# Kernel tuning notes

Measured on AMD Instinct MI355X. Metric: run time of the kernel, lower is better.

## Reference

```python
import jax, jax.numpy as jnp
import numpy as np

N = 100000   # nodes
F = 512      # in_channels
H = 128      # hidden_channels
HEADS = 2
E = 1600000  # edges
C = 64       # out_channels (classes)
EPS = 1e-5
GW = 0.8     # graph_weight


def setup_inputs() -> dict:
    key = jax.random.key(0)
    ks = jax.random.split(key, 16)
    rn = lambda k, s: jax.random.normal(k, s, jnp.float32) * 0.05
    return {
        'x': jax.random.normal(ks[0], (N, F), jnp.float32),
        'edge_index': jax.random.randint(ks[1], (2, E), 0, N),
        # TransConv params
        't_fc_w': rn(ks[2], (F, H)), 't_fc_b': jnp.zeros((H,), jnp.float32),
        't_ln0_g': jnp.ones((H,), jnp.float32), 't_ln0_b': jnp.zeros((H,), jnp.float32),
        't_wq_w': rn(ks[3], (H, H * HEADS)), 't_wq_b': jnp.zeros((H * HEADS,), jnp.float32),
        't_wk_w': rn(ks[4], (H, H * HEADS)), 't_wk_b': jnp.zeros((H * HEADS,), jnp.float32),
        't_wv_w': rn(ks[5], (H, H * HEADS)), 't_wv_b': jnp.zeros((H * HEADS,), jnp.float32),
        't_ln1_g': jnp.ones((H,), jnp.float32), 't_ln1_b': jnp.zeros((H,), jnp.float32),
        # GraphConv params
        'g_fc_w': rn(ks[6], (F, H)), 'g_fc_b': jnp.zeros((H,), jnp.float32),
        'g_bn0_g': jnp.ones((H,), jnp.float32), 'g_bn0_b': jnp.zeros((H,), jnp.float32),
        'g_conv_w': rn(ks[7], (H, H)), 'g_conv_b': jnp.zeros((H,), jnp.float32),
        'g_bn1_g': jnp.ones((H,), jnp.float32), 'g_bn1_b': jnp.zeros((H,), jnp.float32),
        # output fc
        'fc_w': rn(ks[8], (H, C)), 'fc_b': jnp.zeros((C,), jnp.float32),
    }


def _layernorm(x, g, b):
    mu = jnp.mean(x, axis=-1, keepdims=True)
    var = jnp.mean((x - mu) ** 2, axis=-1, keepdims=True)
    return (x - mu) * jax.lax.rsqrt(var + EPS) * g + b


def _batchnorm_eval(x, g, b):
    # eval-mode BN right after reset: running_mean=0, running_var=1
    return x * (1.0 / np.sqrt(1.0 + EPS)) * g + b


def _trans_conv(x, fc_w, fc_b, ln0_g, ln0_b, wq_w, wq_b, wk_w, wk_b, wv_w, wv_b, ln1_g, ln1_b):
    h = jax.nn.relu(_layernorm(x @ fc_w + fc_b, ln0_g, ln0_b))
    x0 = h
    n = h.shape[0]
    qs = (h @ wq_w + wq_b).reshape(n, HEADS, H)
    ks = (h @ wk_w + wk_b).reshape(n, HEADS, H)
    vs = (h @ wv_w + wv_b).reshape(n, HEADS, H)
    # global (Frobenius) norm, as in torch.norm(qs, p=2)
    qs = qs / jnp.linalg.norm(qs)
    ks = ks / jnp.linalg.norm(ks)
    kvs = jnp.einsum('lhm,lhd->hmd', ks, vs)                  # [h, m, d]
    attention_num = jnp.einsum('nhm,hmd->nhd', qs, kvs) + n * vs
    ks_sum = jnp.sum(ks, axis=0)                              # [h, m]
    normalizer = jnp.einsum('nhm,hm->nh', qs, ks_sum)[..., None] + float(n)
    attn_out = (attention_num / normalizer).mean(axis=1)       # [n, H]
    h = (attn_out + x0) / 2.0
    h = jax.nn.relu(_layernorm(h, ln1_g, ln1_b))
    return h


def _graph_conv(x, edge_index, fc_w, fc_b, bn0_g, bn0_b, conv_w, conv_b, bn1_g, bn1_b):
    h = jax.nn.relu(_batchnorm_eval(x @ fc_w + fc_b, bn0_g, bn0_b))
    x0 = h
    row, col = edge_index[0], edge_index[1]
    n = h.shape[0]
    deg = jax.ops.segment_sum(jnp.ones((row.shape[0],), jnp.float32), col, num_segments=n)
    val = jnp.sqrt(1.0 / deg[col]) * jnp.sqrt(1.0 / deg[row])
    val = jnp.nan_to_num(val, nan=0.0, posinf=0.0, neginf=0.0)
    agg = jax.ops.segment_sum(val[:, None] * h[row], col, num_segments=n)  # [n, H]
    h2 = agg @ conv_w + conv_b
    h2 = jax.nn.relu(_batchnorm_eval(h2, bn1_g, bn1_b))
    return h2 + x0


def reference(x, edge_index,
              t_fc_w, t_fc_b, t_ln0_g, t_ln0_b, t_wq_w, t_wq_b, t_wk_w, t_wk_b,
              t_wv_w, t_wv_b, t_ln1_g, t_ln1_b,
              g_fc_w, g_fc_b, g_bn0_g, g_bn0_b, g_conv_w, g_conv_b, g_bn1_g, g_bn1_b,
              fc_w, fc_b):
    x1 = _trans_conv(x, t_fc_w, t_fc_b, t_ln0_g, t_ln0_b, t_wq_w, t_wq_b,
                     t_wk_w, t_wk_b, t_wv_w, t_wv_b, t_ln1_g, t_ln1_b)
    x2 = _graph_conv(x, edge_index, g_fc_w, g_fc_b, g_bn0_g, g_bn0_b,
                     g_conv_w, g_conv_b, g_bn1_g, g_bn1_b)
    out = GW * x2 + (1.0 - GW) * x1
    return out @ fc_w + fc_b
```

## Files before the change

kernel.cpp:

```cpp
#include <hip/hip_runtime.h>

constexpr int N = 100000;
constexpr int F = 512;
constexpr int H = 128;
constexpr int E = 1600000;
constexpr int C = 64;
constexpr float EPS = 1e-5f;
constexpr float NF = 100000.0f;
constexpr float IBN = 0.999995000037f;

constexpr size_t OFF_HT   = 0;
constexpr size_t OFF_HG   = 12800000;
constexpr size_t OFF_AGG  = 25600000;
constexpr size_t OFF_CNT  = 38400000;
constexpr size_t OFF_S    = 38500000;
constexpr size_t OFF_G    = 38500128;
constexpr size_t OFF_PTR  = 38516512;
constexpr size_t OFF_CUR  = 38616512;
constexpr size_t OFF_BS   = 38716512;
constexpr size_t OFF_SROW = 38716640;
constexpr size_t OFF_SVAL = 40316640;
constexpr size_t OFF_GWV  = 41916640;
constexpr size_t OFF_KV   = OFF_GWV + 3 * 32768;
constexpr size_t OFF_KSUM = OFF_KV + 32768;
constexpr size_t OFF_VSUM = OFF_KSUM + 256;
constexpr size_t OFF_QSUM = OFF_VSUM + 256;
constexpr size_t OFF_SC   = OFF_QSUM + 256;
constexpr size_t OFF_B    = OFF_SC + 4;
constexpr size_t OFF_CC   = OFF_B + 32768;
constexpr size_t OFF_U    = OFF_CC + 256;
constexpr size_t OFF_U0   = OFF_U + 256;
constexpr size_t OFF_BT   = OFF_U0 + 4;

constexpr int NB1024 = (N + 1023) / 1024;
constexpr int NB_GRAM = (N + 255) / 256;
constexpr size_t SP_BASE = (size_t)NB_GRAM * 16384;

typedef __attribute__((ext_vector_type(8))) short short8;
typedef __attribute__((ext_vector_type(4))) float floatx4;

__device__ __forceinline__ float4 ld4(const float* p) {
  return *reinterpret_cast<const float4*>(p);
}
__device__ __forceinline__ void st4(float* p, float4 v) {
  *reinterpret_cast<float4*>(p) = v;
}
__device__ __forceinline__ unsigned short f2bf(float f) {
  unsigned u = __float_as_uint(f);
  u += 0x7fff + ((u >> 16) & 1);
  return (unsigned short)(u >> 16);
}
__device__ __forceinline__ float bf2f(unsigned short h) {
  return __uint_as_float((unsigned)h << 16);
}
__device__ __forceinline__ void gl_lds16(const unsigned short* g, unsigned short* l) {
  __builtin_amdgcn_global_load_lds(
      (const __attribute__((address_space(1))) unsigned int*)g,
      (__attribute__((address_space(3))) unsigned int*)l, 16, 0, 0);
}

__global__ __launch_bounds__(256) void k0_cvt(const float* __restrict__ Wt,
    const float* __restrict__ Wg, unsigned short* __restrict__ Bt)
{
  const int idx = blockIdx.x * 256 + threadIdx.x;
  const int k = idx >> 8;
  const int n = idx & 255;
  float v = (n < 128) ? Wt[(size_t)k * H + n] : Wg[(size_t)k * H + (n - 128)];
  const int kt = k >> 5;
  const int g  = (k >> 3) & 3;
  const int e  = k & 7;
  const int chunk = g * 256 + ((n + 2 * g) & 255);
  Bt[(((size_t)kt * 1024 + chunk) << 3) + e] = f2bf(v);
}

__global__ __launch_bounds__(256, 3) void k1_mfma(
    const float* __restrict__ x, const unsigned short* __restrict__ Bt,
    const float* __restrict__ bt, const float* __restrict__ lng, const float* __restrict__ lnb,
    const float* __restrict__ bgv, const float* __restrict__ bng, const float* __restrict__ bnb,
    float* __restrict__ ht, float* __restrict__ hg)
{
  __shared__ __align__(16) union {
    struct { unsigned short A[2][64 * 40]; unsigned short B[2][8192]; } st;
    struct { float lns[64 * 132]; float mu[64]; float rs[64]; } ln;
  } sm;
  const int t = threadIdx.x;
  const int lane = t & 63;
  const int w = t >> 6;
  const int rq = (w >> 1) * 32;
  const int cq = (w & 1) * 128;
  const int g = lane >> 4;
  const int m = lane & 15;
  const int M0 = blockIdx.x * 64;

  floatx4 acc[2][8];
#pragma unroll
  for (int rt = 0; rt < 2; ++rt)
#pragma unroll
    for (int ct = 0; ct < 8; ++ct) acc[rt][ct] = (floatx4){0.f, 0.f, 0.f, 0.f};

  const int srow = t >> 2;
  const int scol8 = (t & 3) * 8;
  const int grow = (M0 + srow < N) ? (M0 + srow) : (N - 1);
  const float* xp = x + (size_t)grow * F + scol8;

  const int mb = cq + m + 2 * g;

  {
#pragma unroll
    for (int i = 0; i < 4; ++i)
      gl_lds16(Bt + (((size_t)(i * 256 + t)) << 3),
               &sm.st.B[0][(size_t)(i * 256 + (w << 6)) << 3]);
    float4 a0 = ld4(xp), a1 = ld4(xp + 4);
    ushort4 p0, p1;
    p0.x = f2bf(a0.x); p0.y = f2bf(a0.y); p0.z = f2bf(a0.z); p0.w = f2bf(a0.w);
    p1.x = f2bf(a1.x); p1.y = f2bf(a1.y); p1.z = f2bf(a1.z); p1.w = f2bf(a1.w);
    *(ushort4*)(sm.st.A[0] + srow * 40 + scol8) = p0;
    *(ushort4*)(sm.st.A[0] + srow * 40 + scol8 + 4) = p1;
  }
  __syncthreads();

#pragma unroll 2
  for (int kt = 0; kt < 16; ++kt) {
    const int cur = kt & 1, nxt = cur ^ 1;
    float4 a0, a1;
    const bool more = (kt + 1 < 16);
    if (more) {
#pragma unroll
      for (int i = 0; i < 4; ++i)
        gl_lds16(Bt + (((size_t)(kt + 1) * 1024 + i * 256 + t) << 3),
                 &sm.st.B[nxt][(size_t)(i * 256 + (w << 6)) << 3]);
      a0 = ld4(xp + (kt + 1) * 32);
      a1 = ld4(xp + (kt + 1) * 32 + 4);
    }
    {
      const unsigned short* Ab = sm.st.A[cur];
      const unsigned short* Bb = sm.st.B[cur];
      short8 af[2], bf[8];
#pragma unroll
      for (int rt = 0; rt < 2; ++rt)
        af[rt] = *(const short8*)(Ab + (rq + rt * 16 + m) * 40 + g * 8);
#pragma unroll
      for (int ct = 0; ct < 8; ++ct) {
        const int chunk = g * 256 + ((mb + ct * 16) & 255);
        bf[ct] = *(const short8*)(Bb + ((size_t)chunk << 3));
      }
#pragma unroll
      for (int rt = 0; rt < 2; ++rt)
#pragma unroll
        for (int ct = 0; ct < 8; ++ct)
          acc[rt][ct] = __builtin_amdgcn_mfma_f32_16x16x32_bf16(af[rt], bf[ct], acc[rt][ct], 0, 0, 0);
    }
    if (more) {
      ushort4 p0, p1;
      p0.x = f2bf(a0.x); p0.y = f2bf(a0.y); p0.z = f2bf(a0.z); p0.w = f2bf(a0.w);
      p1.x = f2bf(a1.x); p1.y = f2bf(a1.y); p1.z = f2bf(a1.z); p1.w = f2bf(a1.w);
      *(ushort4*)(sm.st.A[nxt] + srow * 40 + scol8) = p0;
      *(ushort4*)(sm.st.A[nxt] + srow * 40 + scol8 + 4) = p1;
    }
    __syncthreads();
  }

  if (cq == 0) {
#pragma unroll
    for (int rt = 0; rt < 2; ++rt)
#pragma unroll
      for (int ct = 0; ct < 8; ++ct) {
        const int col = ct * 16 + m;
        const float b = bt[col];
#pragma unroll
        for (int r = 0; r < 4; ++r)
          sm.ln.lns[(rq + rt * 16 + g * 4 + r) * 132 + col] = acc[rt][ct][r] + b;
      }
  } else {
#pragma unroll
    for (int rt = 0; rt < 2; ++rt)
#pragma unroll
      for (int ct = 0; ct < 8; ++ct) {
        const int col = ct * 16 + m;
        const float s1 = IBN * bng[col], b0 = bgv[col], b2 = bnb[col];
#pragma unroll
        for (int r = 0; r < 4; ++r) {
          const int row = M0 + rq + rt * 16 + g * 4 + r;
          if (row < N) {
            float v = (acc[rt][ct][r] + b0) * s1 + b2;
            hg[(size_t)row * H + col] = v > 0.f ? v : 0.f;
          }
        }
      }
  }
  __syncthreads();
  if (t < 64) {
    float sum = 0.f, sq = 0.f;
    for (int c2 = 0; c2 < H; ++c2) {
      float v = sm.ln.lns[t * 132 + c2];
      sum += v; sq += v * v;
    }
    float mu = sum * (1.f / H);
    float var = sq * (1.f / H) - mu * mu;
    sm.ln.mu[t] = mu; sm.ln.rs[t] = rsqrtf(var + EPS);
  }
  __syncthreads();
  {
    const int r = t >> 2;
    const int cb = (t & 3) * 32;
    if (M0 + r < N) {
      const float mu = sm.ln.mu[r], rs = sm.ln.rs[r];
#pragma unroll
      for (int j = 0; j < 8; ++j) {
        const int c = cb + j * 4;
        float o[4];
#pragma unroll
        for (int q = 0; q < 4; ++q) {
          float v = (sm.ln.lns[r * 132 + c + q] - mu) * rs * lng[c + q] + lnb[c + q];
          o[q] = v > 0.f ? v : 0.f;
        }
        st4(ht + (size_t)(M0 + r) * H + c, make_float4(o[0], o[1], o[2], o[3]));
      }
    }
  }
}

__global__ __launch_bounds__(256) void k2_gram(const float* __restrict__ ht,
                                               float* __restrict__ gp,
                                               float* __restrict__ sp)
{
  const int t = threadIdx.x;
  const int b = blockIdx.x;
  const int base = b * 256;
  const int nend = (base + 256 < N) ? base + 256 : N;
  const int r0 = (t >> 4) * 8;
  const int c0 = (t & 15) * 8;
  float acc[8][8] = {};
  float colacc[8] = {};
  const bool do_col = (t < 16);
  int n = base;
  for (; n + 1 < nend; n += 2) {
    const float* hp0 = ht + (size_t)n * H;
    const float* hp1 = hp0 + H;
    float4 a00 = ld4(hp0 + r0), a01 = ld4(hp0 + r0 + 4);
    float4 b00 = ld4(hp0 + c0), b01 = ld4(hp0 + c0 + 4);
    float4 a10 = ld4(hp1 + r0), a11 = ld4(hp1 + r0 + 4);
    float4 b10 = ld4(hp1 + c0), b11 = ld4(hp1 + c0 + 4);
    float a0[8] = {a00.x, a00.y, a00.z, a00.w, a01.x, a01.y, a01.z, a01.w};
    float b0[8] = {b00.x, b00.y, b00.z, b00.w, b01.x, b01.y, b01.z, b01.w};
    float a1[8] = {a10.x, a10.y, a10.z, a10.w, a11.x, a11.y, a11.z, a11.w};
    float b1[8] = {b10.x, b10.y, b10.z, b10.w, b11.x, b11.y, b11.z, b11.w};
    if (do_col) {
#pragma unroll
      for (int j = 0; j < 8; ++j) colacc[j] += b0[j] + b1[j];
    }
#pragma unroll
    for (int i = 0; i < 8; ++i)
#pragma unroll
      for (int j = 0; j < 8; ++j)
        acc[i][j] += a0[i] * b0[j] + a1[i] * b1[j];
  }
  if (n < nend) {
    const float* hp0 = ht + (size_t)n * H;
    float4 a00 = ld4(hp0 + r0), a01 = ld4(hp0 + r0 + 4);
    float4 b00 = ld4(hp0 + c0), b01 = ld4(hp0 + c0 + 4);
    float a0[8] = {a00.x, a00.y, a00.z, a00.w, a01.x, a01.y, a01.z, a01.w};
    float b0[8] = {b00.x, b00.y, b00.z, b00.w, b01.x, b01.y, b01.z, b01.w};
    if (do_col) {
#pragma unroll
      for (int j = 0; j < 8; ++j) colacc[j] += b0[j];
    }
#pragma unroll
    for (int i = 0; i < 8; ++i)
#pragma unroll
      for (int j = 0; j < 8; ++j)
        acc[i][j] += a0[i] * b0[j];
  }
  float* g = gp + (size_t)b * 16384;
#pragma unroll
  for (int i = 0; i < 8; ++i) {
    st4(&g[(r0 + i) * H + c0], make_float4(acc[i][0], acc[i][1], acc[i][2], acc[i][3]));
    st4(&g[(r0 + i) * H + c0 + 4], make_float4(acc[i][4], acc[i][5], acc[i][6], acc[i][7]));
  }
  if (do_col) {
    float* spb = sp + (size_t)b * 128;
    st4(&spb[c0], make_float4(colacc[0], colacc[1], colacc[2], colacc[3]));
    st4(&spb[c0 + 4], make_float4(colacc[4], colacc[5], colacc[6], colacc[7]));
  }
}

__global__ __launch_bounds__(256) void k2r_reduce(const float* __restrict__ gp,
    const float* __restrict__ sp, float* __restrict__ G, float* __restrict__ s)
{
  const int i = blockIdx.x * 256 + threadIdx.x;
  float s0 = 0.f, s1 = 0.f, s2 = 0.f, s3 = 0.f;
  int b = 0;
  for (; b + 3 < NB_GRAM; b += 4) {
    s0 += gp[(size_t)b * 16384 + i];
    s1 += gp[(size_t)(b + 1) * 16384 + i];
    s2 += gp[(size_t)(b + 2) * 16384 + i];
    s3 += gp[(size_t)(b + 3) * 16384 + i];
  }
  for (; b < NB_GRAM; ++b) s0 += gp[(size_t)b * 16384 + i];
  G[i] = (s0 + s1) + (s2 + s3);
  if (blockIdx.x == 0 && threadIdx.x < 128) {
    float t0 = 0.f, t1 = 0.f;
    int bb = 0;
    for (; bb + 1 < NB_GRAM; bb += 2) {
      t0 += sp[(size_t)bb * 128 + threadIdx.x];
      t1 += sp[(size_t)(bb + 1) * 128 + threadIdx.x];
    }
    for (; bb < NB_GRAM; ++bb) t0 += sp[(size_t)bb * 128 + threadIdx.x];
    s[threadIdx.x] = t0 + t1;
  }
}

__global__ __launch_bounds__(256) void k3a_gw(const float* __restrict__ G,
    const float* __restrict__ Wv, const float* __restrict__ Wk,
    const float* __restrict__ Wq, float* __restrict__ GW)
{
  const int flat = blockIdx.x * 256 + threadIdx.x;
  const int w = flat >> 15;
  const int rem = flat & 32767;
  const int i = rem >> 8;
  const int j = rem & 255;
  const float* W = (w == 0) ? Wv : (w == 1) ? Wk : Wq;
  float sum = 0.f;
#pragma unroll 8
  for (int k = 0; k < H; ++k) sum += G[i * H + k] * W[k * 256 + j];
  GW[flat] = sum;
}

__global__ __launch_bounds__(256) void k3k_sums(const float* __restrict__ s,
    const float* __restrict__ Wk, const float* __restrict__ bk,
    const float* __restrict__ Wv, const float* __restrict__ bv,
    const float* __restrict__ Wq, const float* __restrict__ bq,
    float* __restrict__ ksum, float* __restrict__ vsum, float* __restrict__ qsum)
{
  const int flat = blockIdx.x * 256 + threadIdx.x;
  const int w = flat >> 8;
  const int j = flat & 255;
  const float* W = (w == 0) ? Wk : (w == 1) ? Wv : Wq;
  const float* b = (w == 0) ? bk : (w == 1) ? bv : bq;
  float* out = (w == 0) ? ksum : (w == 1) ? vsum : qsum;
  float sum = 0.f;
#pragma unroll 8
  for (int k = 0; k < H; ++k) sum += s[k] * W[k * 256 + j];
  out[j] = sum + NF * b[j];
}

__global__ __launch_bounds__(256) void k3b_kv(const float* __restrict__ GWv,
    const float* __restrict__ s, const float* __restrict__ Wk,
    const float* __restrict__ bk, const float* __restrict__ bv,
    const float* __restrict__ vsum, float* __restrict__ kv)
{
  const int flat = blockIdx.x * 256 + threadIdx.x;
  const int h = flat >> 14;
  const int m = (flat >> 7) & 127;
  const int d = flat & 127;
  float s1 = 0.f, s2 = 0.f;
#pragma unroll 4
  for (int k = 0; k < H; ++k) {
    float wkv = Wk[k * 256 + h * 128 + m];
    s1 += wkv * GWv[k * 256 + h * 128 + d];
    s2 += wkv * s[k];
  }
  kv[flat] = s1 + s2 * bv[h * 128 + d] + bk[h * 128 + m] * vsum[h * 128 + d];
}

__global__ __launch_bounds__(256) void k3c_ssq(
    const float* __restrict__ Wk, const float* __restrict__ GWk,
    const float* __restrict__ Wq, const float* __restrict__ GWq,
    const float* __restrict__ bk, const float* __restrict__ ksum,
    const float* __restrict__ bq, const float* __restrict__ qsum,
    float* __restrict__ sc)
{
  __shared__ float red[512];
  const int t = threadIdx.x;
  float pk = 0.f, pq = 0.f;
  for (int i = t; i < 32768; i += 256) {
    pk += Wk[i] * GWk[i];
    pq += Wq[i] * GWq[i];
  }
  pk += 2.f * bk[t] * ksum[t] - NF * bk[t] * bk[t];
  pq += 2.f * bq[t] * qsum[t] - NF * bq[t] * bq[t];
  red[t] = pk; red[256 + t] = pq;
  __syncthreads();
  for (int off = 128; off > 0; off >>= 1) {
    if (t < off) { red[t] += red[t + off]; red[256 + t] += red[256 + t + off]; }
    __syncthreads();
  }
  if (t == 0) {
    float ssq_k = red[0], ssq_q = red[256];
    sc[0] = ssq_q; sc[1] = ssq_k;
    sc[2] = rsqrtf(ssq_q * ssq_k);
  }
}

__global__ __launch_bounds__(256) void k3d_B(const float* __restrict__ Wq,
    const float* __restrict__ kv, const float* __restrict__ Wv,
    const float* __restrict__ sc, unsigned short* __restrict__ Bt2)
{
  const int flat = blockIdx.x * 256 + threadIdx.x;
  const int i = flat >> 8;
  const int j = flat & 255;
  const int h = j >> 7;
  const int d = j & 127;
  const float inv = sc[2];
  float sum = 0.f;
#pragma unroll 4
  for (int m = 0; m < H; ++m)
    sum += Wq[i * 256 + h * 128 + m] * kv[h * 16384 + m * 128 + d];
  Bt2[(size_t)j * H + i] = f2bf(sum * inv + NF * Wv[i * 256 + j]);
}

__global__ __launch_bounds__(512) void k3e_small(const float* __restrict__ bq,
    const float* __restrict__ kv, const float* __restrict__ bv,
    const float* __restrict__ Wq, const float* __restrict__ ksum,
    const float* __restrict__ sc, float* __restrict__ cc,
    float* __restrict__ u, float* __restrict__ u0)
{
  const int t = threadIdx.x;
  const float inv = sc[2];
  if (t < 256) {
    const int h = t >> 7, d = t & 127;
    float sum = 0.f;
    for (int m = 0; m < H; ++m) sum += bq[h * 128 + m] * kv[h * 16384 + m * 128 + d];
    cc[t] = sum * inv + NF * bv[t];
  } else {
    const int q = t - 256;
    const int i = q >> 1, h = q & 1;
    float sum = 0.f;
    for (int m = 0; m < H; ++m) sum += Wq[i * 256 + h * 128 + m] * ksum[h * 128 + m];
    u[i * 2 + h] = sum * inv;
  }
  if (t < 2) {
    float sum = 0.f;
    for (int m = 0; m < H; ++m) sum += bq[t * 128 + m] * ksum[t * 128 + m];
    u0[t] = sum * inv + NF;
  }
}

__global__ __launch_bounds__(256) void k4_mfma(float* __restrict__ ht,
    const unsigned short* __restrict__ Bt2, const float* __restrict__ cc,
    const float* __restrict__ u, const float* __restrict__ u0,
    const float* __restrict__ lng, const float* __restrict__ lnb)
{
  __shared__ __align__(16) union {
    unsigned short A[64 * 136];
    float lns[64 * 132];
  } sm;
  __shared__ float u_s[256];
  __shared__ float rden_s[128];
  __shared__ float mu_s[64], rs_s[64];
  const int t = threadIdx.x;
  const int lane = t & 63;
  const int w = t >> 6;
  const int rq = w * 16;
  const int g = lane >> 4;
  const int m = lane & 15;
  const int M0 = blockIdx.x * 64;

  {
    const int srow = t >> 2;
    const int scol = (t & 3) * 32;
    const int grow = (M0 + srow < N) ? (M0 + srow) : (N - 1);
    const float* xp = ht + (size_t)grow * H + scol;
#pragma unroll
    for (int j = 0; j < 8; ++j) {
      float4 a4 = ld4(xp + j * 4);
      ushort4 p;
      p.x = f2bf(a4.x); p.y = f2bf(a4.y); p.z = f2bf(a4.z); p.w = f2bf(a4.w);
      *(ushort4*)(sm.A + srow * 136 + scol + j * 4) = p;
    }
  }
  u_s[t] = u[t];
  __syncthreads();

  floatx4 acc[16];
#pragma unroll
  for (int ct = 0; ct < 16; ++ct) acc[ct] = (floatx4){0.f, 0.f, 0.f, 0.f};
#pragma unroll
  for (int kk = 0; kk < 128; kk += 32) {
    short8 af = *(const short8*)(sm.A + (rq + m) * 136 + kk + g * 8);
#pragma unroll
    for (int ct = 0; ct < 16; ++ct) {
      short8 bf = *(const short8*)(Bt2 + (size_t)(ct * 16 + m) * H + kk + g * 8);
      acc[ct] = __builtin_amdgcn_mfma_f32_16x16x32_bf16(af, bf, acc[ct], 0, 0, 0);
    }
  }
  if (t < 128) {
    const int row = t >> 1, head = t & 1;
    float den = u0[head];
    for (int k = 0; k < H; ++k)
      den += bf2f(sm.A[row * 136 + k]) * u_s[k * 2 + head];
    rden_s[row * 2 + head] = 0.5f / den;
  }
  __syncthreads();

#pragma unroll
  for (int ct = 0; ct < 8; ++ct) {
    const int d = ct * 16 + m;
    const float c0v = cc[d], c1v = cc[128 + d];
#pragma unroll
    for (int r = 0; r < 4; ++r) {
      const int row = rq + g * 4 + r;
      const int grow = M0 + row;
      const float rd0 = rden_s[row * 2], rd1 = rden_s[row * 2 + 1];
      float attn = (acc[ct][r] + c0v) * rd0 + (acc[ct + 8][r] + c1v) * rd1;
      float hres = (grow < N) ? ht[(size_t)grow * H + d] : 0.f;
      sm.lns[row * 132 + d] = (attn + hres) * 0.5f;
    }
  }
  __syncthreads();
  if (t < 64) {
    float sum = 0.f, sq = 0.f;
    for (int c2 = 0; c2 < H; ++c2) {
      float v = sm.lns[t * 132 + c2];
      sum += v; sq += v * v;
    }
    float mu = sum * (1.f / H);
    float var = sq * (1.f / H) - mu * mu;
    mu_s[t] = mu; rs_s[t] = rsqrtf(var + EPS);
  }
  __syncthreads();
  {
    const int r = t >> 2;
    const int cb = (t & 3) * 32;
    if (M0 + r < N) {
      const float mu = mu_s[r], rs = rs_s[r];
#pragma unroll
      for (int j = 0; j < 8; ++j) {
        const int c = cb + j * 4;
        float o[4];
#pragma unroll
        for (int q = 0; q < 4; ++q) {
          float v = (sm.lns[r * 132 + c + q] - mu) * rs * lng[c + q] + lnb[c + q];
          o[q] = v > 0.f ? v : 0.f;
        }
        st4(ht + (size_t)(M0 + r) * H + c, make_float4(o[0], o[1], o[2], o[3]));
      }
    }
  }
}

__global__ __launch_bounds__(256) void k5_deg(const int* __restrict__ ei,
                                              int* __restrict__ cnt)
{
  const int i = blockIdx.x * 256 + threadIdx.x;
  if (i < E) atomicAdd(&cnt[ei[E + i]], 1);
}

__global__ __launch_bounds__(256) void k_scan1(const int* __restrict__ cnt,
                                               int* __restrict__ bsum)
{
  __shared__ int red[256];
  const int t = threadIdx.x;
  const int base = blockIdx.x * 1024 + t * 4;
  int s = 0;
#pragma unroll
  for (int j = 0; j < 4; ++j) {
    int idx = base + j;
    if (idx < N) s += cnt[idx];
  }
  red[t] = s;
  __syncthreads();
  for (int off = 128; off > 0; off >>= 1) {
    if (t < off) red[t] += red[t + off];
    __syncthreads();
  }
  if (t == 0) bsum[blockIdx.x] = red[0];
}

__global__ void k_scan2(int* __restrict__ bsum)
{
  if (threadIdx.x == 0 && blockIdx.x == 0) {
    int run = 0;
    for (int b = 0; b < NB1024; ++b) {
      int v = bsum[b];
      bsum[b] = run;
      run += v;
    }
  }
}

__global__ __launch_bounds__(256) void k_scan3(const int* __restrict__ cnt,
    const int* __restrict__ bsum, int* __restrict__ ptr, int* __restrict__ cur)
{
  __shared__ int part[256];
  const int t = threadIdx.x;
  const int base = blockIdx.x * 1024 + t * 4;
  int v[4];
  int tsum = 0;
#pragma unroll
  for (int j = 0; j < 4; ++j) {
    int idx = base + j;
    v[j] = (idx < N) ? cnt[idx] : 0;
    tsum += v[j];
  }
  part[t] = tsum;
  __syncthreads();
  for (int off = 1; off < 256; off <<= 1) {
    int add = (t >= off) ? part[t - off] : 0;
    __syncthreads();
    part[t] += add;
    __syncthreads();
  }
  int run = bsum[blockIdx.x] + part[t] - tsum;
#pragma unroll
  for (int j = 0; j < 4; ++j) {
    int idx = base + j;
    if (idx < N) { ptr[idx] = run; cur[idx] = run; }
    run += v[j];
  }
}

__global__ __launch_bounds__(256) void k6a_place(const int* __restrict__ ei,
    const int* __restrict__ cnt, int* __restrict__ cur,
    int* __restrict__ srow, float* __restrict__ sval)
{
  const int e = blockIdx.x * 256 + threadIdx.x;
  if (e >= E) return;
  const int r = ei[e];
  const int c = ei[E + e];
  const int p = atomicAdd(&cur[c], 1);
  srow[p] = r;
  const int dr = cnt[r];
  const float dv = (float)dr * (float)cnt[c];
  sval[p] = (dr > 0) ? rsqrtf(dv) : 0.f;
}

__global__ __launch_bounds__(256) void k6b_gather(const int* __restrict__ ptr,
    const int* __restrict__ cnt, const int* __restrict__ srow,
    const float* __restrict__ sval, const float* __restrict__ hg,
    float* __restrict__ agg)
{
  const int t = threadIdx.x;
  const int n = blockIdx.x * 8 + (t >> 5);
  const int lane4 = (t & 31) * 4;
  const int start = ptr[n];
  const int end = start + cnt[n];
  float4 acc = make_float4(0.f, 0.f, 0.f, 0.f);
  int e = start;
  for (; e + 1 < end; e += 2) {
    int r0 = srow[e], r1 = srow[e + 1];
    float v0 = sval[e], v1 = sval[e + 1];
    float4 h0 = ld4(hg + (size_t)r0 * H + lane4);
    float4 h1 = ld4(hg + (size_t)r1 * H + lane4);
    acc.x += v0 * h0.x + v1 * h1.x;
    acc.y += v0 * h0.y + v1 * h1.y;
    acc.z += v0 * h0.z + v1 * h1.z;
    acc.w += v0 * h0.w + v1 * h1.w;
  }
  if (e < end) {
    int r0 = srow[e];
    float v0 = sval[e];
    float4 h0 = ld4(hg + (size_t)r0 * H + lane4);
    acc.x += v0 * h0.x;
    acc.y += v0 * h0.y;
    acc.z += v0 * h0.z;
    acc.w += v0 * h0.w;
  }
  st4(agg + (size_t)n * H + lane4, acc);
}

__global__ __launch_bounds__(256) void k7_conv(const float* __restrict__ agg,
    float* __restrict__ hg, const float* __restrict__ Wc,
    const float* __restrict__ cb, const float* __restrict__ g1,
    const float* __restrict__ b1)
{
  const int t = threadIdx.x;
  const int R0 = blockIdx.x * 32;
  const int r0 = (t >> 5) * 4;
  const int c0 = (t & 31) * 4;
  float acc[4][4] = {};
  for (int k0 = 0; k0 < H; k0 += 4) {
    float ax[4][4];
#pragma unroll
    for (int r = 0; r < 4; ++r) {
      float4 a4 = ld4(agg + (size_t)(R0 + r0 + r) * H + k0);
      ax[r][0] = a4.x; ax[r][1] = a4.y; ax[r][2] = a4.z; ax[r][3] = a4.w;
    }
#pragma unroll
    for (int kk = 0; kk < 4; ++kk) {
      float4 w = ld4(Wc + (size_t)(k0 + kk) * H + c0);
#pragma unroll
      for (int r = 0; r < 4; ++r) {
        float av = ax[r][kk];
        acc[r][0] += av * w.x; acc[r][1] += av * w.y;
        acc[r][2] += av * w.z; acc[r][3] += av * w.w;
      }
    }
  }
#pragma unroll
  for (int r = 0; r < 4; ++r) {
    size_t off = (size_t)(R0 + r0 + r) * H + c0;
    float4 res = ld4(hg + off);
    float rsv[4] = {res.x, res.y, res.z, res.w};
    float o[4];
#pragma unroll
    for (int j = 0; j < 4; ++j) {
      float v = (acc[r][j] + cb[c0 + j]) * IBN * g1[c0 + j] + b1[c0 + j];
      v = v > 0.f ? v : 0.f;
      o[j] = v + rsv[j];
    }
    st4(hg + off, make_float4(o[0], o[1], o[2], o[3]));
  }
}

__global__ __launch_bounds__(256) void k8_out(const float* __restrict__ ht,
    const float* __restrict__ hg, const float* __restrict__ W,
    const float* __restrict__ bias, float* __restrict__ out)
{
  const int t = threadIdx.x;
  const int R0 = blockIdx.x * 32;
  const int rr0 = (t >> 4) * 2;
  const int c0 = (t & 15) * 4;
  float acc[2][4] = {};
  for (int k0 = 0; k0 < H; k0 += 4) {
    float ax[2][4];
#pragma unroll
    for (int r = 0; r < 2; ++r) {
      size_t off = (size_t)(R0 + rr0 + r) * H + k0;
      float4 a1 = ld4(ht + off);
      float4 a2 = ld4(hg + off);
      ax[r][0] = 0.2f * a1.x + 0.8f * a2.x;
      ax[r][1] = 0.2f * a1.y + 0.8f * a2.y;
      ax[r][2] = 0.2f * a1.z + 0.8f * a2.z;
      ax[r][3] = 0.2f * a1.w + 0.8f * a2.w;
    }
#pragma unroll
    for (int kk = 0; kk < 4; ++kk) {
      float4 w = ld4(W + (size_t)(k0 + kk) * C + c0);
#pragma unroll
      for (int r = 0; r < 2; ++r) {
        float av = ax[r][kk];
        acc[r][0] += av * w.x; acc[r][1] += av * w.y;
        acc[r][2] += av * w.z; acc[r][3] += av * w.w;
      }
    }
  }
#pragma unroll
  for (int r = 0; r < 2; ++r) {
    float o[4];
#pragma unroll
    for (int j = 0; j < 4; ++j) o[j] = acc[r][j] + bias[c0 + j];
    st4(out + (size_t)(R0 + rr0 + r) * C + c0, make_float4(o[0], o[1], o[2], o[3]));
  }
}

extern "C" void kernel_launch(void* const* d_in, const int* in_sizes, int n_in,
                              void* d_out, int out_size, void* d_ws, size_t ws_size,
                              hipStream_t stream) {
  (void)in_sizes; (void)n_in; (void)out_size; (void)ws_size;
  const float* x       = (const float*)d_in[0];
  const int*   ei      = (const int*)d_in[1];
  const float* t_fc_w  = (const float*)d_in[2];
  const float* t_fc_b  = (const float*)d_in[3];
  const float* t_ln0_g = (const float*)d_in[4];
  const float* t_ln0_b = (const float*)d_in[5];
  const float* t_wq_w  = (const float*)d_in[6];
  const float* t_wq_b  = (const float*)d_in[7];
  const float* t_wk_w  = (const float*)d_in[8];
  const float* t_wk_b  = (const float*)d_in[9];
  const float* t_wv_w  = (const float*)d_in[10];
  const float* t_wv_b  = (const float*)d_in[11];
  const float* t_ln1_g = (const float*)d_in[12];
  const float* t_ln1_b = (const float*)d_in[13];
  const float* g_fc_w  = (const float*)d_in[14];
  const float* g_fc_b  = (const float*)d_in[15];
  const float* g_bn0_g = (const float*)d_in[16];
  const float* g_bn0_b = (const float*)d_in[17];
  const float* g_cv_w  = (const float*)d_in[18];
  const float* g_cv_b  = (const float*)d_in[19];
  const float* g_bn1_g = (const float*)d_in[20];
  const float* g_bn1_b = (const float*)d_in[21];
  const float* fc_w    = (const float*)d_in[22];
  const float* fc_b    = (const float*)d_in[23];

  float* W    = (float*)d_ws;
  float* ht   = W + OFF_HT;
  float* hg   = W + OFF_HG;
  float* agg  = W + OFF_AGG;
  int*   cnt  = (int*)(W + OFF_CNT);
  float* s    = W + OFF_S;
  float* G    = W + OFF_G;
  int*   ptr  = (int*)(W + OFF_PTR);
  int*   cur  = (int*)(W + OFF_CUR);
  int*   bsum = (int*)(W + OFF_BS);
  int*   srow = (int*)(W + OFF_SROW);
  float* sval = W + OFF_SVAL;
  float* gw   = W + OFF_GWV;
  float* kv   = W + OFF_KV;
  float* ksum = W + OFF_KSUM;
  float* vsum = W + OFF_VSUM;
  float* qsum = W + OFF_QSUM;
  float* sc   = W + OFF_SC;
  unsigned short* Bt2 = (unsigned short*)(W + OFF_B);
  float* cc   = W + OFF_CC;
  float* u    = W + OFF_U;
  float* u0   = W + OFF_U0;
  unsigned short* Bt = (unsigned short*)(W + OFF_BT);

  hipMemsetAsync(cnt, 0, N * sizeof(int), stream);

  k0_cvt<<<512, 256, 0, stream>>>(t_fc_w, g_fc_w, Bt);

  k5_deg<<<(E + 255) / 256, 256, 0, stream>>>(ei, cnt);
  k_scan1<<<NB1024, 256, 0, stream>>>(cnt, bsum);
  k_scan2<<<1, 64, 0, stream>>>(bsum);
  k_scan3<<<NB1024, 256, 0, stream>>>(cnt, bsum, ptr, cur);
  k6a_place<<<E / 256, 256, 0, stream>>>(ei, cnt, cur, srow, sval);

  k1_mfma<<<(N + 63) / 64, 256, 0, stream>>>(x, Bt, t_fc_b, t_ln0_g, t_ln0_b,
                                             g_fc_b, g_bn0_g, g_bn0_b, ht, hg);
  k2_gram<<<NB_GRAM, 256, 0, stream>>>(ht, agg, agg + SP_BASE);
  k2r_reduce<<<64, 256, 0, stream>>>(agg, agg + SP_BASE, G, s);
  k6b_gather<<<N / 8, 256, 0, stream>>>(ptr, cnt, srow, sval, hg, agg);
  k3a_gw<<<384, 256, 0, stream>>>(G, t_wv_w, t_wk_w, t_wq_w, gw);
  k3k_sums<<<3, 256, 0, stream>>>(s, t_wk_w, t_wk_b, t_wv_w, t_wv_b, t_wq_w, t_wq_b,
                                  ksum, vsum, qsum);
  k3b_kv<<<128, 256, 0, stream>>>(gw, s, t_wk_w, t_wk_b, t_wv_b, vsum, kv);
  k3c_ssq<<<1, 256, 0, stream>>>(t_wk_w, gw + 32768, t_wq_w, gw + 65536,
                                 t_wk_b, ksum, t_wq_b, qsum, sc);
  k3d_B<<<128, 256, 0, stream>>>(t_wq_w, kv, t_wv_w, sc, Bt2);
  k3e_small<<<1, 512, 0, stream>>>(t_wq_b, kv, t_wv_b, t_wq_w, ksum, sc, cc, u, u0);
  k4_mfma<<<(N + 63) / 64, 256, 0, stream>>>(ht, Bt2, cc, u, u0, t_ln1_g, t_ln1_b);
  k7_conv<<<N / 32, 256, 0, stream>>>(agg, hg, g_cv_w, g_cv_b, g_bn1_g, g_bn1_b);
  k8_out<<<N / 32, 256, 0, stream>>>(ht, hg, fc_w, fc_b, (float*)d_out);
}
```

Measured before the change: 1.172 ms.

## Triple-buffer K-loop of fc GEMM with manual waitcnt and MFMA priority

Changes the k1_mfma main loop from double to triple buffering of the A and B LDS tiles. Loads now run two K-steps ahead, and fine-grained s_waitcnt/s_barrier replace __syncthreads. s_setprio raises wave priority around the MFMA block, and occupancy is lowered to 2 blocks per SM to make room for the extra LDS. The aim is to hide global-load latency better in the input projection GEMM, at the cost of occupancy and of correctness resting on hand-written vmcnt counts.

```diff
diff --git a/kernel.cpp b/kernel.cpp
--- a/kernel.cpp
+++ b/kernel.cpp
@@ -73,14 +73,14 @@
   Bt[(((size_t)kt * 1024 + chunk) << 3) + e] = f2bf(v);
 }
 
-__global__ __launch_bounds__(256, 3) void k1_mfma(
+__global__ __launch_bounds__(256, 2) void k1_mfma(
     const float* __restrict__ x, const unsigned short* __restrict__ Bt,
     const float* __restrict__ bt, const float* __restrict__ lng, const float* __restrict__ lnb,
     const float* __restrict__ bgv, const float* __restrict__ bng, const float* __restrict__ bnb,
     float* __restrict__ ht, float* __restrict__ hg)
 {
   __shared__ __align__(16) union {
-    struct { unsigned short A[2][64 * 40]; unsigned short B[2][8192]; } st;
+    struct { unsigned short A[3][64 * 40]; unsigned short B[3][8192]; } st;
     struct { float lns[64 * 132]; float mu[64]; float rs[64]; } ln;
   } sm;
   const int t = threadIdx.x;
@@ -105,36 +105,56 @@
 
   const int mb = cq + m + 2 * g;
 
+  unsigned short* const Abase = &sm.st.A[0][0];
+  unsigned short* const Bbase = &sm.st.B[0][0];
+  const int ldsw = (w << 6);
+
+  float4 a0, a1;
+
   {
 #pragma unroll
     for (int i = 0; i < 4; ++i)
       gl_lds16(Bt + (((size_t)(i * 256 + t)) << 3),
-               &sm.st.B[0][(size_t)(i * 256 + (w << 6)) << 3]);
-    float4 a0 = ld4(xp), a1 = ld4(xp + 4);
-    ushort4 p0, p1;
+               Bbase + ((size_t)(i * 256 + ldsw) << 3));
+    a0 = ld4(xp); a1 = ld4(xp + 4);
+    asm volatile("s_waitcnt vmcnt(0)" ::: "memory");
+    ushort4 p0, p1v;
     p0.x = f2bf(a0.x); p0.y = f2bf(a0.y); p0.z = f2bf(a0.z); p0.w = f2bf(a0.w);
-    p1.x = f2bf(a1.x); p1.y = f2bf(a1.y); p1.z = f2bf(a1.z); p1.w = f2bf(a1.w);
-    *(ushort4*)(sm.st.A[0] + srow * 40 + scol8) = p0;
-    *(ushort4*)(sm.st.A[0] + srow * 40 + scol8 + 4) = p1;
-  }
-  __syncthreads();
-
-#pragma unroll 2
-  for (int kt = 0; kt < 16; ++kt) {
-    const int cur = kt & 1, nxt = cur ^ 1;
-    float4 a0, a1;
-    const bool more = (kt + 1 < 16);
-    if (more) {
+    p1v.x = f2bf(a1.x); p1v.y = f2bf(a1.y); p1v.z = f2bf(a1.z); p1v.w = f2bf(a1.w);
+    *(ushort4*)(Abase + srow * 40 + scol8) = p0;
+    *(ushort4*)(Abase + srow * 40 + scol8 + 4) = p1v;
+#pragma unroll
+    for (int i = 0; i < 4; ++i)
+      gl_lds16(Bt + (((size_t)1024 + i * 256 + t) << 3),
+               Bbase + 8192 + ((size_t)(i * 256 + ldsw) << 3));
+    a0 = ld4(xp + 32); a1 = ld4(xp + 36);
+    asm volatile("s_waitcnt lgkmcnt(0)\ns_barrier" ::: "memory");
+  }
+
+  int bc = 0, b1 = 1, b2 = 2;
+  for (int kt = 0; kt < 14; ++kt) {
+    {
+      unsigned short* Bn = Bbase + b2 * 8192;
 #pragma unroll
       for (int i = 0; i < 4; ++i)
-        gl_lds16(Bt + (((size_t)(kt + 1) * 1024 + i * 256 + t) << 3),
-                 &sm.st.B[nxt][(size_t)(i * 256 + (w << 6)) << 3]);
-      a0 = ld4(xp + (kt + 1) * 32);
-      a1 = ld4(xp + (kt + 1) * 32 + 4);
-    }
+        gl_lds16(Bt + (((size_t)(kt + 2) * 1024 + i * 256 + t) << 3),
+                 Bn + ((size_t)(i * 256 + ldsw) << 3));
+    }
+    asm volatile("s_waitcnt vmcnt(4)" ::: "memory");
     {
-      const unsigned short* Ab = sm.st.A[cur];
-      const unsigned short* Bb = sm.st.B[cur];
+      ushort4 p0, p1v;
+      p0.x = f2bf(a0.x); p0.y = f2bf(a0.y); p0.z = f2bf(a0.z); p0.w = f2bf(a0.w);
+      p1v.x = f2bf(a1.x); p1v.y = f2bf(a1.y); p1v.z = f2bf(a1.z); p1v.w = f2bf(a1.w);
+      unsigned short* An = Abase + b1 * 2560;
+      *(ushort4*)(An + srow * 40 + scol8) = p0;
+      *(ushort4*)(An + srow * 40 + scol8 + 4) = p1v;
+    }
+    a0 = ld4(xp + (kt + 2) * 32);
+    a1 = ld4(xp + (kt + 2) * 32 + 4);
+    asm volatile("s_waitcnt lgkmcnt(0)\ns_barrier" ::: "memory");
+    {
+      const unsigned short* Ab = Abase + bc * 2560;
+      const unsigned short* Bb = Bbase + bc * 8192;
       short8 af[2], bf[8];
 #pragma unroll
       for (int rt = 0; rt < 2; ++rt)
@@ -144,21 +164,49 @@
         const int chunk = g * 256 + ((mb + ct * 16) & 255);
         bf[ct] = *(const short8*)(Bb + ((size_t)chunk << 3));
       }
+      __builtin_amdgcn_s_setprio(1);
 #pragma unroll
       for (int rt = 0; rt < 2; ++rt)
 #pragma unroll
         for (int ct = 0; ct < 8; ++ct)
           acc[rt][ct] = __builtin_amdgcn_mfma_f32_16x16x32_bf16(af[rt], bf[ct], acc[rt][ct], 0, 0, 0);
-    }
-    if (more) {
-      ushort4 p0, p1;
-      p0.x = f2bf(a0.x); p0.y = f2bf(a0.y); p0.z = f2bf(a0.z); p0.w = f2bf(a0.w);
-      p1.x = f2bf(a1.x); p1.y = f2bf(a1.y); p1.z = f2bf(a1.z); p1.w = f2bf(a1.w);
-      *(ushort4*)(sm.st.A[nxt] + srow * 40 + scol8) = p0;
-      *(ushort4*)(sm.st.A[nxt] + srow * 40 + scol8 + 4) = p1;
-    }
-    __syncthreads();
-  }
+      __builtin_amdgcn_s_setprio(0);
+    }
+    const int tmp = bc; bc = b1; b1 = b2; b2 = tmp;
+  }
+  {
+    asm volatile("s_waitcnt vmcnt(0)" ::: "memory");
+    ushort4 p0, p1v;
+    p0.x = f2bf(a0.x); p0.y = f2bf(a0.y); p0.z = f2bf(a0.z); p0.w = f2bf(a0.w);
+    p1v.x = f2bf(a1.x); p1v.y = f2bf(a1.y); p1v.z = f2bf(a1.z); p1v.w = f2bf(a1.w);
+    unsigned short* An = Abase + b1 * 2560;
+    *(ushort4*)(An + srow * 40 + scol8) = p0;
+    *(ushort4*)(An + srow * 40 + scol8 + 4) = p1v;
+    asm volatile("s_waitcnt lgkmcnt(0)\ns_barrier" ::: "memory");
+#pragma unroll
+    for (int step = 0; step < 2; ++step) {
+      const int bi = (step == 0) ? bc : b1;
+      const unsigned short* Ab = Abase + bi * 2560;
+      const unsigned short* Bb = Bbase + bi * 8192;
+      short8 af[2], bf[8];
+#pragma unroll
+      for (int rt = 0; rt < 2; ++rt)
+        af[rt] = *(const short8*)(Ab + (rq + rt * 16 + m) * 40 + g * 8);
+#pragma unroll
+      for (int ct = 0; ct < 8; ++ct) {
+        const int chunk = g * 256 + ((mb + ct * 16) & 255);
+        bf[ct] = *(const short8*)(Bb + ((size_t)chunk << 3));
+      }
+      __builtin_amdgcn_s_setprio(1);
+#pragma unroll
+      for (int rt = 0; rt < 2; ++rt)
+#pragma unroll
+        for (int ct = 0; ct < 8; ++ct)
+          acc[rt][ct] = __builtin_amdgcn_mfma_f32_16x16x32_bf16(af[rt], bf[ct], acc[rt][ct], 0, 0, 0);
+      __builtin_amdgcn_s_setprio(0);
+    }
+  }
+  __syncthreads();
 
   if (cq == 0) {
 #pragma unroll
@@ -177,12 +225,12 @@
 #pragma unroll
       for (int ct = 0; ct < 8; ++ct) {
         const int col = ct * 16 + m;
-        const float s1 = IBN * bng[col], b0 = bgv[col], b2 = bnb[col];
+        const float s1 = IBN * bng[col], b0 = bgv[col], b2v = bnb[col];
 #pragma unroll
         for (int r = 0; r < 4; ++r) {
           const int row = M0 + rq + rt * 16 + g * 4 + r;
           if (row < N) {
-            float v = (acc[rt][ct][r] + b0) * s1 + b2;
+            float v = (acc[rt][ct][r] + b0) * s1 + b2v;
             hg[(size_t)row * H + col] = v > 0.f ? v : 0.f;
           }
         }
```

Result: slower. 1.199 ms (+2.3%).

## Enlarge k1 tile to 128 rows, fuse LayerNorm into registers, parallelize scan2

Applied to the files above, without the earlier changes.

The first GEMM kernel now uses 512-thread blocks covering 128 rows, so each staged B tile is shared by twice as many rows and half as many blocks are launched. The LayerNorm epilogue is computed directly from the MFMA accumulators with cross-lane shuffles, replacing the shared-memory staging pass that ran a serial row reduction on only 64 threads. The single-thread block-sum scan becomes a 128-thread parallel Hillis-Steele scan. In exchange, the ht stores become strided scalar writes instead of float4 writes, and the larger block with more LDS may lower occupancy.

```diff
diff --git a/kernel.cpp b/kernel.cpp
--- a/kernel.cpp
+++ b/kernel.cpp
@@ -73,15 +73,15 @@
   Bt[(((size_t)kt * 1024 + chunk) << 3) + e] = f2bf(v);
 }
 
-__global__ __launch_bounds__(256, 3) void k1_mfma(
+__global__ __launch_bounds__(512, 4) void k1_mfma(
     const float* __restrict__ x, const unsigned short* __restrict__ Bt,
     const float* __restrict__ bt, const float* __restrict__ lng, const float* __restrict__ lnb,
     const float* __restrict__ bgv, const float* __restrict__ bng, const float* __restrict__ bnb,
     float* __restrict__ ht, float* __restrict__ hg)
 {
-  __shared__ __align__(16) union {
-    struct { unsigned short A[2][64 * 40]; unsigned short B[2][8192]; } st;
-    struct { float lns[64 * 132]; float mu[64]; float rs[64]; } ln;
+  __shared__ __align__(16) struct {
+    unsigned short A[2][128 * 40];
+    unsigned short B[2][8192];
   } sm;
   const int t = threadIdx.x;
   const int lane = t & 63;
@@ -90,7 +90,7 @@
   const int cq = (w & 1) * 128;
   const int g = lane >> 4;
   const int m = lane & 15;
-  const int M0 = blockIdx.x * 64;
+  const int M0 = blockIdx.x * 128;
 
   floatx4 acc[2][8];
 #pragma unroll
@@ -104,18 +104,19 @@
   const float* xp = x + (size_t)grow * F + scol8;
 
   const int mb = cq + m + 2 * g;
+  const int ldsw = (w << 6);
 
   {
 #pragma unroll
-    for (int i = 0; i < 4; ++i)
-      gl_lds16(Bt + (((size_t)(i * 256 + t)) << 3),
-               &sm.st.B[0][(size_t)(i * 256 + (w << 6)) << 3]);
+    for (int i = 0; i < 2; ++i)
+      gl_lds16(Bt + (((size_t)(i * 512 + t)) << 3),
+               &sm.B[0][(size_t)(i * 512 + ldsw) << 3]);
     float4 a0 = ld4(xp), a1 = ld4(xp + 4);
     ushort4 p0, p1;
     p0.x = f2bf(a0.x); p0.y = f2bf(a0.y); p0.z = f2bf(a0.z); p0.w = f2bf(a0.w);
     p1.x = f2bf(a1.x); p1.y = f2bf(a1.y); p1.z = f2bf(a1.z); p1.w = f2bf(a1.w);
-    *(ushort4*)(sm.st.A[0] + srow * 40 + scol8) = p0;
-    *(ushort4*)(sm.st.A[0] + srow * 40 + scol8 + 4) = p1;
+    *(ushort4*)(sm.A[0] + srow * 40 + scol8) = p0;
+    *(ushort4*)(sm.A[0] + srow * 40 + scol8 + 4) = p1;
   }
   __syncthreads();
 
@@ -126,15 +127,15 @@
     const bool more = (kt + 1 < 16);
     if (more) {
 #pragma unroll
-      for (int i = 0; i < 4; ++i)
-        gl_lds16(Bt + (((size_t)(kt + 1) * 1024 + i * 256 + t) << 3),
-                 &sm.st.B[nxt][(size_t)(i * 256 + (w << 6)) << 3]);
+      for (int i = 0; i < 2; ++i)
+        gl_lds16(Bt + (((size_t)(kt + 1) * 1024 + i * 512 + t) << 3),
+                 &sm.B[nxt][(size_t)(i * 512 + ldsw) << 3]);
       a0 = ld4(xp + (kt + 1) * 32);
       a1 = ld4(xp + (kt + 1) * 32 + 4);
     }
     {
-      const unsigned short* Ab = sm.st.A[cur];
-      const unsigned short* Bb = sm.st.B[cur];
+      const unsigned short* Ab = sm.A[cur];
+      const unsigned short* Bb = sm.B[cur];
       short8 af[2], bf[8];
 #pragma unroll
       for (int rt = 0; rt < 2; ++rt)
@@ -154,67 +155,64 @@
       ushort4 p0, p1;
       p0.x = f2bf(a0.x); p0.y = f2bf(a0.y); p0.z = f2bf(a0.z); p0.w = f2bf(a0.w);
       p1.x = f2bf(a1.x); p1.y = f2bf(a1.y); p1.z = f2bf(a1.z); p1.w = f2bf(a1.w);
-      *(ushort4*)(sm.st.A[nxt] + srow * 40 + scol8) = p0;
-      *(ushort4*)(sm.st.A[nxt] + srow * 40 + scol8 + 4) = p1;
+      *(ushort4*)(sm.A[nxt] + srow * 40 + scol8) = p0;
+      *(ushort4*)(sm.A[nxt] + srow * 40 + scol8 + 4) = p1;
     }
     __syncthreads();
   }
 
   if (cq == 0) {
-#pragma unroll
-    for (int rt = 0; rt < 2; ++rt)
-#pragma unroll
-      for (int ct = 0; ct < 8; ++ct) {
-        const int col = ct * 16 + m;
-        const float b = bt[col];
-#pragma unroll
-        for (int r = 0; r < 4; ++r)
-          sm.ln.lns[(rq + rt * 16 + g * 4 + r) * 132 + col] = acc[rt][ct][r] + b;
+    float bt_l[8], lng_l[8], lnb_l[8];
+#pragma unroll
+    for (int ct = 0; ct < 8; ++ct) {
+      bt_l[ct] = bt[ct * 16 + m];
+      lng_l[ct] = lng[ct * 16 + m];
+      lnb_l[ct] = lnb[ct * 16 + m];
+    }
+#pragma unroll
+    for (int rt = 0; rt < 2; ++rt) {
+#pragma unroll
+      for (int r = 0; r < 4; ++r) {
+        float sum = 0.f, sq = 0.f;
+#pragma unroll
+        for (int ct = 0; ct < 8; ++ct) {
+          float v = acc[rt][ct][r] + bt_l[ct];
+          acc[rt][ct][r] = v;
+          sum += v; sq += v * v;
+        }
+#pragma unroll
+        for (int off = 1; off < 16; off <<= 1) {
+          sum += __shfl_xor(sum, off, 64);
+          sq  += __shfl_xor(sq,  off, 64);
+        }
+        const float mu = sum * (1.f / H);
+        const float rs = rsqrtf(sq * (1.f / H) - mu * mu + EPS);
+        const int row = M0 + rq + rt * 16 + g * 4 + r;
+        if (row < N) {
+          float* hp = ht + (size_t)row * H + m;
+#pragma unroll
+          for (int ct = 0; ct < 8; ++ct) {
+            float o = (acc[rt][ct][r] - mu) * rs * lng_l[ct] + lnb_l[ct];
+            hp[ct * 16] = o > 0.f ? o : 0.f;
+          }
+        }
       }
+    }
   } else {
 #pragma unroll
-    for (int rt = 0; rt < 2; ++rt)
-#pragma unroll
-      for (int ct = 0; ct < 8; ++ct) {
-        const int col = ct * 16 + m;
-        const float s1 = IBN * bng[col], b0 = bgv[col], b2 = bnb[col];
+    for (int ct = 0; ct < 8; ++ct) {
+      const int c2 = ct * 16 + m;
+      const float s1 = IBN * bng[c2], b0 = bgv[c2], b2v = bnb[c2];
+#pragma unroll
+      for (int rt = 0; rt < 2; ++rt) {
 #pragma unroll
         for (int r = 0; r < 4; ++r) {
           const int row = M0 + rq + rt * 16 + g * 4 + r;
           if (row < N) {
-            float v = (acc[rt][ct][r] + b0) * s1 + b2;
-            hg[(size_t)row * H + col] = v > 0.f ? v : 0.f;
+            float v = (acc[rt][ct][r] + b0) * s1 + b2v;
+            hg[(size_t)row * H + c2] = v > 0.f ? v : 0.f;
           }
         }
-      }
-  }
-  __syncthreads();
-  if (t < 64) {
-    float sum = 0.f, sq = 0.f;
-    for (int c2 = 0; c2 < H; ++c2) {
-      float v = sm.ln.lns[t * 132 + c2];
-      sum += v; sq += v * v;
-    }
-    float mu = sum * (1.f / H);
-    float var = sq * (1.f / H) - mu * mu;
-    sm.ln.mu[t] = mu; sm.ln.rs[t] = rsqrtf(var + EPS);
-  }
-  __syncthreads();
-  {
-    const int r = t >> 2;
-    const int cb = (t & 3) * 32;
-    if (M0 + r < N) {
-      const float mu = sm.ln.mu[r], rs = sm.ln.rs[r];
-#pragma unroll
-      for (int j = 0; j < 8; ++j) {
-        const int c = cb + j * 4;
-        float o[4];
-#pragma unroll
-        for (int q = 0; q < 4; ++q) {
-          float v = (sm.ln.lns[r * 132 + c + q] - mu) * rs * lng[c + q] + lnb[c + q];
-          o[q] = v > 0.f ? v : 0.f;
-        }
-        st4(ht + (size_t)(M0 + r) * H + c, make_float4(o[0], o[1], o[2], o[3]));
       }
     }
   }
@@ -567,16 +565,20 @@
   if (t == 0) bsum[blockIdx.x] = red[0];
 }
 
-__global__ void k_scan2(int* __restrict__ bsum)
-{
-  if (threadIdx.x == 0 && blockIdx.x == 0) {
-    int run = 0;
-    for (int b = 0; b < NB1024; ++b) {
-      int v = bsum[b];
-      bsum[b] = run;
-      run += v;
-    }
-  }
+__global__ __launch_bounds__(128) void k_scan2(int* __restrict__ bsum)
+{
+  __shared__ int sh[128];
+  const int t = threadIdx.x;
+  const int v = (t < NB1024) ? bsum[t] : 0;
+  sh[t] = v;
+  __syncthreads();
+  for (int off = 1; off < 128; off <<= 1) {
+    int add = (t >= off) ? sh[t - off] : 0;
+    __syncthreads();
+    sh[t] += add;
+    __syncthreads();
+  }
+  if (t < NB1024) bsum[t] = sh[t] - v;
 }
 
 __global__ __launch_bounds__(256) void k_scan3(const int* __restrict__ cnt,
@@ -803,12 +805,12 @@
 
   k5_deg<<<(E + 255) / 256, 256, 0, stream>>>(ei, cnt);
   k_scan1<<<NB1024, 256, 0, stream>>>(cnt, bsum);
-  k_scan2<<<1, 64, 0, stream>>>(bsum);
+  k_scan2<<<1, 128, 0, stream>>>(bsum);
   k_scan3<<<NB1024, 256, 0, stream>>>(cnt, bsum, ptr, cur);
   k6a_place<<<E / 256, 256, 0, stream>>>(ei, cnt, cur, srow, sval);
 
-  k1_mfma<<<(N + 63) / 64, 256, 0, stream>>>(x, Bt, t_fc_b, t_ln0_g, t_ln0_b,
-                                             g_fc_b, g_bn0_g, g_bn0_b, ht, hg);
+  k1_mfma<<<(N + 127) / 128, 512, 0, stream>>>(x, Bt, t_fc_b, t_ln0_g, t_ln0_b,
+                                               g_fc_b, g_bn0_g, g_bn0_b, ht, hg);
   k2_gram<<<NB_GRAM, 256, 0, stream>>>(ht, agg, agg + SP_BASE);
   k2r_reduce<<<64, 256, 0, stream>>>(agg, agg + SP_BASE, G, s);
   k6b_gather<<<N / 8, 256, 0, stream>>>(ptr, cnt, srow, sval, hg, agg);
```

New measurement: 1.145 ms. 2.3% less time.
